# Kernel optimization log

Measured on AMD Instinct MI355X. Metric: run time of the kernel, lower is better.

The kernel has to match this reference:

```python
import jax, jax.numpy as jnp
import numpy as np

B, V, E = 2, 50000, 400000
FIN, COND, HID, OUT, ENC, EDG = 128, 32, 256, 128, 64, 16
EPS = 1e-5


def setup_inputs() -> dict:
    key = jax.random.key(0)
    ks = jax.random.split(key, 24)
    rn = lambda k, shp, s=0.05: jax.random.normal(k, shp, jnp.float32) * s
    return {
        "x": jax.random.normal(ks[0], (B, V, FIN), jnp.float32),
        "cond_x": jax.random.normal(ks[1], (V, COND), jnp.float32),
        "edge_attr": jax.random.normal(ks[2], (E, EDG), jnp.float32),
        "t": jax.random.normal(ks[3], (B, ENC), jnp.float32),
        "edge_index": jax.random.randint(ks[4], (2, E), 0, V, dtype=jnp.int32),
        # GCNConv weights (in, hid) + bias; Linear weights (hid, out) + bias
        "w_c0": rn(ks[5], (FIN + COND, HID)), "b_c0": rn(ks[6], (HID,)),
        "w_l0": rn(ks[7], (HID, HID)), "b_l0": rn(ks[8], (HID,)),
        "w_c1": rn(ks[9], (HID, HID)), "b_c1": rn(ks[10], (HID,)),
        "w_l1": rn(ks[11], (HID, HID)), "b_l1": rn(ks[12], (HID,)),
        "w_c2": rn(ks[13], (HID, HID)), "b_c2": rn(ks[14], (HID,)),
        "w_l2": rn(ks[15], (HID, OUT)), "b_l2": rn(ks[16], (OUT,)),
        "gn_g": jnp.ones((HID,), jnp.float32), "gn_b": jnp.zeros((HID,), jnp.float32),
        "film_w": rn(ks[17], (ENC, 2 * HID)), "film_b": rn(ks[18], (2 * HID,)),
    }


def _gcn(h, src, dst, dinv, W, b):
    # GCNConv: symmetric-normalized aggregation with self loops, then +bias.
    hw = h @ W  # (B, V, H)
    coef = (dinv[src] * dinv[dst])[None, :, None]            # (1, E, 1)
    self_loop = hw * (dinv * dinv)[None, :, None]            # norm of (i,i) edge
    agg = self_loop.at[:, dst, :].add(hw[:, src, :] * coef)  # scatter-add over dst
    return agg + b


def _groupnorm1(h, gamma, beta):
    # nn.GroupNorm(1, C) applied to (B, C, V): normalize over (C, V) per sample.
    mu = h.mean(axis=(1, 2), keepdims=True)
    var = ((h - mu) ** 2).mean(axis=(1, 2), keepdims=True)
    return (h - mu) * jax.lax.rsqrt(var + EPS) * gamma + beta


def reference(x, cond_x, edge_attr, t, edge_index,
              w_c0, b_c0, w_l0, b_l0, w_c1, b_c1, w_l1, b_l1,
              w_c2, b_c2, w_l2, b_l2, gn_g, gn_b, film_w, film_b):
    src, dst = edge_index[0], edge_index[1]
    deg = jnp.ones((V,), jnp.float32).at[dst].add(1.0)  # 1 = self loop
    dinv = jax.lax.rsqrt(deg)

    x_skip = x
    cond = jnp.broadcast_to(cond_x[None], (x.shape[0], V, COND))
    h = jnp.concatenate([x, cond], axis=-1)  # (B, V, FIN+COND)

    # layer 0: feature dim != hidden -> no norm
    h = jax.nn.relu(_gcn(h, src, dst, dinv, w_c0, b_c0))
    h = jax.nn.relu(h @ w_l0 + b_l0)  # dropout p=0 -> identity

    # layer 1: GroupNorm(1, hidden) then conv/linear
    h = _groupnorm1(h, gn_g, gn_b)
    h = jax.nn.relu(_gcn(h, src, dst, dinv, w_c1, b_c1))
    h = jax.nn.relu(h @ w_l1 + b_l1)

    # final gconv + FiLM + relu + linear + residual
    h = _gcn(h, src, dst, dinv, w_c2, b_c2)
    gb = t @ film_w + film_b                 # (B, 2*HID)
    gamma, beta = gb[:, :HID], gb[:, HID:]
    h = h * gamma[:, None, :] + beta[:, None, :]
    h = jax.nn.relu(h)
    out = h @ w_l2 + b_l2 + x_skip
    return out
```

## Files before the change

### kernel.cpp

```cpp
#include <hip/hip_runtime.h>
#include <stdint.h>

typedef unsigned short u16;
typedef short bf16x8 __attribute__((ext_vector_type(8)));
typedef float f32x4 __attribute__((ext_vector_type(4)));

constexpr int B_ = 2, V_ = 50000, E_ = 400000;
constexpr int FIN_ = 128, COND_ = 32, HID_ = 256, OUT_ = 128, ENC_ = 64;
constexpr int M_ = B_ * V_;
constexpr int MP_ = M_ + 256;
constexpr int K0_ = FIN_ + COND_;
constexpr float EPS_ = 1e-5f;

#define DEV static __device__ __forceinline__

DEV float b2f(u16 u) { union { float f; uint32_t i; } x; x.i = ((uint32_t)u) << 16; return x.f; }
DEV u16 f2b(float f) {
  union { float f; uint32_t i; } x; x.f = f;
  uint32_t r = x.i + 0x7fffu + ((x.i >> 16) & 1u);
  return (u16)(r >> 16);
}
DEV uint32_t pk2(float a, float b) { return (uint32_t)f2b(a) | ((uint32_t)f2b(b) << 16); }

#define GLDS16(gp, lp) __builtin_amdgcn_global_load_lds( \
    (const __attribute__((address_space(1))) void*)(gp), \
    (__attribute__((address_space(3))) void*)(lp), 16, 0, 0)

__global__ void k_count(const int* __restrict__ dst, int* __restrict__ cnt) {
  int e = blockIdx.x * blockDim.x + threadIdx.x;
  if (e < E_) atomicAdd(&cnt[dst[e]], 1);
}

__global__ void k_dinv(const int* __restrict__ cnt, float* __restrict__ dinv) {
  int v = blockIdx.x * blockDim.x + threadIdx.x;
  if (v < V_) dinv[v] = rsqrtf(1.0f + (float)cnt[v]);
}

__global__ __launch_bounds__(1024) void k_scan1(const int* __restrict__ cnt,
                                                int* __restrict__ tmp, int* __restrict__ bsum) {
  __shared__ int s[1024];
  int tid = threadIdx.x;
  int i = blockIdx.x * 1024 + tid;
  int v = (i < V_) ? cnt[i] : 0;
  s[tid] = v;
  __syncthreads();
  for (int off = 1; off < 1024; off <<= 1) {
    int t = (tid >= off) ? s[tid - off] : 0;
    __syncthreads();
    s[tid] += t;
    __syncthreads();
  }
  if (i < V_) tmp[i] = s[tid];
  if (tid == 1023) bsum[blockIdx.x] = s[1023];
}

__global__ void k_scan2(int* __restrict__ bsum, int n) {
  if (threadIdx.x == 0) {
    int a = 0;
    for (int i = 0; i < n; ++i) { a += bsum[i]; bsum[i] = a; }
  }
}

__global__ void k_scan3(const int* __restrict__ cnt, const int* __restrict__ tmp,
                        const int* __restrict__ bsum, int* __restrict__ row_ptr,
                        int* __restrict__ cursor) {
  int i = blockIdx.x * blockDim.x + threadIdx.x;
  if (i >= V_) return;
  int blk = i >> 10;
  int offs = blk ? bsum[blk - 1] : 0;
  int incl = tmp[i] + offs;
  row_ptr[i + 1] = incl;
  cursor[i] = incl - cnt[i];
  if (i == 0) row_ptr[0] = 0;
}

__global__ void k_fill(const int* __restrict__ src, const int* __restrict__ dst,
                       const float* __restrict__ dinv,
                       int* __restrict__ cursor, int2* __restrict__ csr) {
  int e = blockIdx.x * blockDim.x + threadIdx.x;
  if (e < E_) {
    int s = src[e], d = dst[e];
    int p = atomicAdd(&cursor[d], 1);
    float cf = dinv[s] * dinv[d];
    csr[p] = make_int2(s, __float_as_int(cf));
  }
}

__global__ void k_rowsum(const float* __restrict__ dinv, const int* __restrict__ row_ptr,
                         const int2* __restrict__ csr, float* __restrict__ rowsum) {
  int v = blockIdx.x * blockDim.x + threadIdx.x;
  if (v >= V_) return;
  float dv = dinv[v];
  float s = dv * dv;
  int e = row_ptr[v + 1];
  for (int j = row_ptr[v]; j < e; ++j) s += __int_as_float(csr[j].y);
  rowsum[v] = s;
}

__global__ void k_film(const float* __restrict__ t, const float* __restrict__ fw,
                       const float* __restrict__ fb, float* __restrict__ gb) {
  int b = blockIdx.x; int j = threadIdx.x;
  float acc = fb[j];
  for (int k = 0; k < ENC_; ++k) acc += t[b * ENC_ + k] * fw[k * 512 + j];
  gb[b * 512 + j] = acc;
}

__global__ void k_wconv(const float* __restrict__ W, u16* __restrict__ WT, int K, int N) {
  int idx = blockIdx.x * blockDim.x + threadIdx.x;
  if (idx < K * N) {
    int k = idx / N, n = idx % N;
    WT[n * K + k] = f2b(W[idx]);
  }
}

__global__ void k_wconv_g(const float* __restrict__ W, const float* __restrict__ gng,
                          u16* __restrict__ WT, int K, int N) {
  int idx = blockIdx.x * blockDim.x + threadIdx.x;
  if (idx < K * N) {
    int k = idx / N, n = idx % N;
    WT[n * K + k] = f2b(W[idx] * gng[k]);
  }
}

__global__ void k_gnreduce(const float4* __restrict__ part, int nblk,
                           float* __restrict__ stats) {
  int tid = threadIdx.x;
  float s0 = 0.f, ss0 = 0.f, s1 = 0.f, ss1 = 0.f;
  for (int i = tid; i < nblk; i += 256) {
    float4 p = part[i];
    s0 += p.x; ss0 += p.y; s1 += p.z; ss1 += p.w;
  }
  __shared__ float red[4][4];
#pragma unroll
  for (int o = 32; o > 0; o >>= 1) {
    s0  += __shfl_down(s0, o, 64);
    ss0 += __shfl_down(ss0, o, 64);
    s1  += __shfl_down(s1, o, 64);
    ss1 += __shfl_down(ss1, o, 64);
  }
  int w = tid >> 6, ln = tid & 63;
  if (ln == 0) { red[w][0] = s0; red[w][1] = ss0; red[w][2] = s1; red[w][3] = ss1; }
  __syncthreads();
  if (tid == 0) {
    float S0 = red[0][0] + red[1][0] + red[2][0] + red[3][0];
    float SS0 = red[0][1] + red[1][1] + red[2][1] + red[3][1];
    float S1 = red[0][2] + red[1][2] + red[2][2] + red[3][2];
    float SS1 = red[0][3] + red[1][3] + red[2][3] + red[3][3];
    float n = (float)V_ * (float)HID_;
    float mu0 = S0 / n, var0 = SS0 / n - mu0 * mu0;
    float mu1 = S1 / n, var1 = SS1 / n - mu1 * mu1;
    stats[0] = mu0; stats[1] = rsqrtf(var0 + EPS_);
    stats[2] = mu1; stats[3] = rsqrtf(var1 + EPS_);
  }
}

__global__ void k_gnfold(const float* __restrict__ gng, const float* __restrict__ gnb,
                         const float* __restrict__ W, const float* __restrict__ stats,
                         float* __restrict__ kc) {
  int n = blockIdx.x, c = threadIdx.x;
  float wv = W[c * HID_ + n];
  float gw = gng[c] * wv, bw = gnb[c] * wv;
  __shared__ float sg[4], sb[4];
#pragma unroll
  for (int o = 32; o > 0; o >>= 1) {
    gw += __shfl_down(gw, o, 64);
    bw += __shfl_down(bw, o, 64);
  }
  int w = c >> 6, ln = c & 63;
  if (ln == 0) { sg[w] = gw; sb[w] = bw; }
  __syncthreads();
  if (c == 0) {
    float G = sg[0] + sg[1] + sg[2] + sg[3];
    float Bw = sb[0] + sb[1] + sb[2] + sb[3];
    for (int b = 0; b < B_; ++b)
      kc[b * HID_ + n] = Bw - stats[b * 2] * stats[b * 2 + 1] * G;
  }
}

__global__ void k_prep0(const float* __restrict__ x, const float* __restrict__ cond,
                        u16* __restrict__ A0) {
  int idx = blockIdx.x * blockDim.x + threadIdx.x;
  if (idx >= M_ * K0_ / 4) return;
  int e = idx * 4;
  int r = e / K0_, c = e % K0_;
  float4 v;
  if (c < FIN_) v = *(const float4*)&x[(size_t)r * FIN_ + c];
  else { int vv = r % V_; v = *(const float4*)&cond[(size_t)vv * COND_ + (c - FIN_)]; }
  uint2 o;
  o.x = pk2(v.x, v.y);
  o.y = pk2(v.z, v.w);
  *(uint2*)&A0[e] = o;
}

template<int KW>
__global__ __launch_bounds__(256) void k_gather(
    const u16* __restrict__ hw, const float* __restrict__ dinv,
    const int* __restrict__ row_ptr, const int2* __restrict__ csr,
    u16* __restrict__ out)
{
  __shared__ f32x4 redA[3][2][32];
  __shared__ f32x4 redB[3][2][32];
  const int v   = blockIdx.x;
  const int tid = threadIdx.x;
  const int nb  = tid >> 6;
  const int b   = (tid >> 5) & 1;
  const int l   = tid & 31;
  const int c0  = l * 8;
  const bool act = l < (KW / 8);

  const float dv = dinv[v];
  const int beg = row_ptr[v], end = row_ptr[v + 1];

  float acc[8];
#pragma unroll
  for (int k = 0; k < 8; ++k) acc[k] = 0.f;

  if (act) {
    int j = beg + nb;
    for (; j + 4 < end; j += 8) {
      int2 e0 = csr[j];
      int2 e1 = csr[j + 4];
      float cf0 = __int_as_float(e0.y);
      float cf1 = __int_as_float(e1.y);
      uint4 u0 = *(const uint4*)&hw[((size_t)b * V_ + e0.x) * KW + c0];
      uint4 u1 = *(const uint4*)&hw[((size_t)b * V_ + e1.x) * KW + c0];
      u16 a0[8]; *(uint4*)a0 = u0;
      u16 a1[8]; *(uint4*)a1 = u1;
#pragma unroll
      for (int k = 0; k < 8; ++k) acc[k] += b2f(a0[k]) * cf0;
#pragma unroll
      for (int k = 0; k < 8; ++k) acc[k] += b2f(a1[k]) * cf1;
    }
    if (j < end) {
      int2 e0 = csr[j];
      float cf0 = __int_as_float(e0.y);
      uint4 u0 = *(const uint4*)&hw[((size_t)b * V_ + e0.x) * KW + c0];
      u16 a0[8]; *(uint4*)a0 = u0;
#pragma unroll
      for (int k = 0; k < 8; ++k) acc[k] += b2f(a0[k]) * cf0;
    }
  }

  if (nb > 0) {
    redA[nb - 1][b][l] = f32x4{acc[0], acc[1], acc[2], acc[3]};
    redB[nb - 1][b][l] = f32x4{acc[4], acc[5], acc[6], acc[7]};
  }
  __syncthreads();
  if (nb == 0 && act) {
#pragma unroll
    for (int g = 0; g < 3; ++g) {
      f32x4 ra = redA[g][b][l], rb = redB[g][b][l];
      acc[0] += ra[0]; acc[1] += ra[1]; acc[2] += ra[2]; acc[3] += ra[3];
      acc[4] += rb[0]; acc[5] += rb[1]; acc[6] += rb[2]; acc[7] += rb[3];
    }
    float sl = dv * dv;
    uint4 u = *(const uint4*)&hw[((size_t)b * V_ + v) * KW + c0];
    u16 us[8]; *(uint4*)us = u;
#pragma unroll
    for (int k = 0; k < 8; ++k) acc[k] += b2f(us[k]) * sl;
    uint4 o;
    o.x = pk2(acc[0], acc[1]);
    o.y = pk2(acc[2], acc[3]);
    o.z = pk2(acc[4], acc[5]);
    o.w = pk2(acc[6], acc[7]);
    *(uint4*)&out[((size_t)b * V_ + v) * KW + c0] = o;
  }
}

template<int P1E, int P2E, int K1, int N2>
__global__ __launch_bounds__(256) void k_pair(
    const u16* __restrict__ A, const u16* __restrict__ W1T, const u16* __restrict__ W2T,
    const float* __restrict__ b1, const float* __restrict__ b2,
    const float* __restrict__ stats, const float* __restrict__ kc,
    const float* __restrict__ rowsum, const float* __restrict__ gb,
    const float* __restrict__ xres, float4* __restrict__ part,
    void* __restrict__ Out)
{
  constexpr int BM = 64, BK = 32, N1 = 256;
  constexpr int FN2 = N2 / 64;
  __shared__ alignas(16) u16 Asg[BM * BK];
  __shared__ alignas(16) u16 Bsg[N1 * BK];
  __shared__ alignas(16) u16 T1[BM * N1];
  __shared__ float sred[4][4];
  const int tile_m = blockIdx.x * BM;
  const int tid = threadIdx.x;
  const int wave = tid >> 6, lane = tid & 63;
  const int lr = lane & 15, lkg = lane >> 4;
  const int phys = lkg ^ ((lr >> 1) & 3);

  f32x4 acc[4][4];
#pragma unroll
  for (int i = 0; i < 4; ++i)
#pragma unroll
    for (int j = 0; j < 4; ++j) acc[i][j] = {0.f, 0.f, 0.f, 0.f};

  for (int kb = 0; kb < K1; kb += BK) {
    {
      int row = tid >> 2;
      int sslot = (tid & 3) ^ ((row >> 1) & 3);
      GLDS16(A + (size_t)(tile_m + row) * K1 + kb + sslot * 8, &Asg[(wave * 64) * 8]);
    }
#pragma unroll
    for (int it = 0; it < 4; ++it) {
      int c = tid + it * 256;
      int row = c >> 2;
      int sslot = (c & 3) ^ ((row >> 1) & 3);
      GLDS16(W1T + (size_t)row * K1 + kb + sslot * 8, &Bsg[(it * 256 + wave * 64) * 8]);
    }
    __syncthreads();
    bf16x8 af[4], bf[4];
#pragma unroll
    for (int fm = 0; fm < 4; ++fm) af[fm] = *(const bf16x8*)&Asg[(fm * 16 + lr) * BK + phys * 8];
#pragma unroll
    for (int fn = 0; fn < 4; ++fn) bf[fn] = *(const bf16x8*)&Bsg[(wave * 64 + fn * 16 + lr) * BK + phys * 8];
#pragma unroll
    for (int fm = 0; fm < 4; ++fm)
#pragma unroll
      for (int fn = 0; fn < 4; ++fn)
        acc[fm][fn] = __builtin_amdgcn_mfma_f32_16x16x32_bf16(bf[fn], af[fm], acc[fm][fn], 0, 0, 0);
    __syncthreads();
  }

#pragma unroll
  for (int fm = 0; fm < 4; ++fm) {
    const int row = fm * 16 + lr;
    const int gr = tile_m + row;
    const int bb = (gr >= V_) ? 1 : 0;
    float rsc = 1.f, rsum = 0.f;
    if (P1E == 1) {
      rsc = stats[bb * 2 + 1];
      int node = (gr < M_) ? (gr - bb * V_) : 0;
      rsum = rowsum[node];
    }
#pragma unroll
    for (int fn = 0; fn < 4; ++fn) {
      const int colb = wave * 64 + fn * 16 + lkg * 4;
      float v0 = acc[fm][fn][0], v1 = acc[fm][fn][1];
      float v2 = acc[fm][fn][2], v3 = acc[fm][fn][3];
      float4 bs = *(const float4*)&b1[colb];
      if (P1E == 0) {
        v0 = fmaxf(v0 + bs.x, 0.f); v1 = fmaxf(v1 + bs.y, 0.f);
        v2 = fmaxf(v2 + bs.z, 0.f); v3 = fmaxf(v3 + bs.w, 0.f);
      }
      if (P1E == 1) {
        float4 kcv = *(const float4*)&kc[bb * 256 + colb];
        v0 = fmaxf(v0 * rsc + rsum * kcv.x + bs.x, 0.f);
        v1 = fmaxf(v1 * rsc + rsum * kcv.y + bs.y, 0.f);
        v2 = fmaxf(v2 * rsc + rsum * kcv.z + bs.z, 0.f);
        v3 = fmaxf(v3 * rsc + rsum * kcv.w + bs.w, 0.f);
      }
      if (P1E == 2) {
        float4 g = *(const float4*)&gb[bb * 512 + colb];
        float4 be = *(const float4*)&gb[bb * 512 + 256 + colb];
        v0 = fmaxf((v0 + bs.x) * g.x + be.x, 0.f);
        v1 = fmaxf((v1 + bs.y) * g.y + be.y, 0.f);
        v2 = fmaxf((v2 + bs.z) * g.z + be.z, 0.f);
        v3 = fmaxf((v3 + bs.w) * g.w + be.w, 0.f);
      }
      int pg = (colb >> 2) ^ ((row & 7) << 1);
      uint2 o; o.x = pk2(v0, v1); o.y = pk2(v2, v3);
      *(uint2*)&T1[row * 256 + pg * 4] = o;
    }
  }
  __syncthreads();

  f32x4 acc2[4][FN2];
#pragma unroll
  for (int i = 0; i < 4; ++i)
#pragma unroll
    for (int j = 0; j < FN2; ++j) acc2[i][j] = {0.f, 0.f, 0.f, 0.f};

  for (int kb2 = 0; kb2 < 256; kb2 += BK) {
#pragma unroll
    for (int it = 0; it < FN2; ++it) {
      int c = tid + it * 256;
      int row = c >> 2;
      int sslot = (c & 3) ^ ((row >> 1) & 3);
      GLDS16(W2T + (size_t)row * 256 + kb2 + sslot * 8, &Bsg[(it * 256 + wave * 64) * 8]);
    }
    __syncthreads();
    bf16x8 af2[4], bf2[FN2];
#pragma unroll
    for (int fm = 0; fm < 4; ++fm) {
      int row = fm * 16 + lr;
      int pg = ((kb2 >> 2) + lkg * 2) ^ ((row & 7) << 1);
      af2[fm] = *(const bf16x8*)&T1[row * 256 + pg * 4];
    }
#pragma unroll
    for (int fn = 0; fn < FN2; ++fn)
      bf2[fn] = *(const bf16x8*)&Bsg[(wave * (N2 / 4) + fn * 16 + lr) * BK + phys * 8];
#pragma unroll
    for (int fm = 0; fm < 4; ++fm)
#pragma unroll
      for (int fn = 0; fn < FN2; ++fn)
        acc2[fm][fn] = __builtin_amdgcn_mfma_f32_16x16x32_bf16(bf2[fn], af2[fm], acc2[fm][fn], 0, 0, 0);
    __syncthreads();
  }

  float s0 = 0.f, ss0 = 0.f, s1 = 0.f, ss1 = 0.f;
#pragma unroll
  for (int fm = 0; fm < 4; ++fm) {
    const int row = tile_m + fm * 16 + lr;
    if (row >= M_) continue;
#pragma unroll
    for (int fn = 0; fn < FN2; ++fn) {
      const int colb = wave * (N2 / 4) + fn * 16 + lkg * 4;
      float v0 = acc2[fm][fn][0], v1 = acc2[fm][fn][1];
      float v2 = acc2[fm][fn][2], v3 = acc2[fm][fn][3];
      float4 bs = *(const float4*)&b2[colb];
      if (P2E == 0 || P2E == 1) {
        v0 = fmaxf(v0 + bs.x, 0.f); v1 = fmaxf(v1 + bs.y, 0.f);
        v2 = fmaxf(v2 + bs.z, 0.f); v3 = fmaxf(v3 + bs.w, 0.f);
        if (P2E == 1) {
          if (row >= V_) { s1 += v0 + v1 + v2 + v3; ss1 += v0*v0 + v1*v1 + v2*v2 + v3*v3; }
          else           { s0 += v0 + v1 + v2 + v3; ss0 += v0*v0 + v1*v1 + v2*v2 + v3*v3; }
        }
        uint2 o; o.x = pk2(v0, v1); o.y = pk2(v2, v3);
        *(uint2*)&((u16*)Out)[(size_t)row * N2 + colb] = o;
      } else {
        float4 xr = *(const float4*)&xres[(size_t)row * N2 + colb];
        float4 o;
        o.x = v0 + bs.x + xr.x; o.y = v1 + bs.y + xr.y;
        o.z = v2 + bs.z + xr.z; o.w = v3 + bs.w + xr.w;
        *(float4*)&((float*)Out)[(size_t)row * N2 + colb] = o;
      }
    }
  }
  if (P2E == 1) {
#pragma unroll
    for (int o = 32; o > 0; o >>= 1) {
      s0  += __shfl_down(s0, o, 64);
      ss0 += __shfl_down(ss0, o, 64);
      s1  += __shfl_down(s1, o, 64);
      ss1 += __shfl_down(ss1, o, 64);
    }
    if (lane == 0) { sred[wave][0] = s0; sred[wave][1] = ss0; sred[wave][2] = s1; sred[wave][3] = ss1; }
    __syncthreads();
    if (tid == 0) {
      float4 p;
      p.x = sred[0][0] + sred[1][0] + sred[2][0] + sred[3][0];
      p.y = sred[0][1] + sred[1][1] + sred[2][1] + sred[3][1];
      p.z = sred[0][2] + sred[1][2] + sred[2][2] + sred[3][2];
      p.w = sred[0][3] + sred[1][3] + sred[2][3] + sred[3][3];
      part[blockIdx.x] = p;
    }
  }
}

extern "C" void kernel_launch(void* const* d_in, const int* in_sizes, int n_in,
                              void* d_out, int out_size, void* d_ws, size_t ws_size,
                              hipStream_t stream) {
  (void)in_sizes; (void)n_in; (void)out_size; (void)ws_size;
  const float* x      = (const float*)d_in[0];
  const float* cond_x = (const float*)d_in[1];
  const float* t      = (const float*)d_in[3];
  const int*   ei     = (const int*)d_in[4];
  const float* w_c0 = (const float*)d_in[5];  const float* b_c0 = (const float*)d_in[6];
  const float* w_l0 = (const float*)d_in[7];  const float* b_l0 = (const float*)d_in[8];
  const float* w_c1 = (const float*)d_in[9];  const float* b_c1 = (const float*)d_in[10];
  const float* w_l1 = (const float*)d_in[11]; const float* b_l1 = (const float*)d_in[12];
  const float* w_c2 = (const float*)d_in[13]; const float* b_c2 = (const float*)d_in[14];
  const float* w_l2 = (const float*)d_in[15]; const float* b_l2 = (const float*)d_in[16];
  const float* gn_g = (const float*)d_in[17]; const float* gn_b = (const float*)d_in[18];
  const float* film_w = (const float*)d_in[19]; const float* film_b = (const float*)d_in[20];

  char* wsp = (char*)d_ws;
  size_t off = 0;
  auto alloc = [&](size_t bytes) -> char* {
    char* p = wsp + off; off += (bytes + 255) & ~(size_t)255; return p;
  };
  constexpr int GM64 = (M_ + 63) / 64;
  int*   cnt       = (int*)  alloc((size_t)V_ * 4);
  int*   row_ptr   = (int*)  alloc((size_t)(V_ + 1) * 4);
  int*   cursor    = (int*)  alloc((size_t)V_ * 4);
  int2*  csr       = (int2*) alloc((size_t)E_ * 8);
  int*   scan_tmp  = (int*)  alloc((size_t)V_ * 4);
  int*   scan_bsum = (int*)  alloc(64 * 4);
  float* dinv      = (float*)alloc((size_t)V_ * 4);
  float* rowsum    = (float*)alloc((size_t)V_ * 4);
  float* stats     = (float*)alloc(16);
  float4* part     = (float4*)alloc((size_t)GM64 * 16);
  float* gb        = (float*)alloc(2 * 512 * 4);
  float* kc        = (float*)alloc(2 * HID_ * 4);
  u16* wc0T  = (u16*)alloc((size_t)256 * 160 * 2);
  u16* wl0T  = (u16*)alloc((size_t)256 * 256 * 2);
  u16* wc1Tg = (u16*)alloc((size_t)256 * 256 * 2);
  u16* wl1T  = (u16*)alloc((size_t)256 * 256 * 2);
  u16* wc2T  = (u16*)alloc((size_t)256 * 256 * 2);
  u16* wl2T  = (u16*)alloc((size_t)128 * 256 * 2);
  u16* A0    = (u16*)alloc((size_t)MP_ * K0_ * 2);
  u16* HA0   = (u16*)alloc((size_t)MP_ * K0_ * 2);
  u16* HB    = (u16*)alloc((size_t)MP_ * HID_ * 2);
  u16* HA1   = (u16*)alloc((size_t)MP_ * HID_ * 2);

  const int* srcI = ei;
  const int* dstI = ei + E_;

  hipMemsetAsync(cnt, 0, (size_t)V_ * 4, stream);

  constexpr int NBLK = (V_ + 1023) / 1024;
  k_count<<<dim3((E_ + 255) / 256), dim3(256), 0, stream>>>(dstI, cnt);
  k_dinv <<<dim3((V_ + 255) / 256), dim3(256), 0, stream>>>(cnt, dinv);
  k_scan1<<<dim3(NBLK), dim3(1024), 0, stream>>>(cnt, scan_tmp, scan_bsum);
  k_scan2<<<dim3(1), dim3(64), 0, stream>>>(scan_bsum, NBLK);
  k_scan3<<<dim3((V_ + 255) / 256), dim3(256), 0, stream>>>(cnt, scan_tmp, scan_bsum, row_ptr, cursor);
  k_fill <<<dim3((E_ + 255) / 256), dim3(256), 0, stream>>>(srcI, dstI, dinv, cursor, csr);
  k_rowsum<<<dim3((V_ + 255) / 256), dim3(256), 0, stream>>>(dinv, row_ptr, csr, rowsum);
  k_film <<<dim3(2), dim3(512), 0, stream>>>(t, film_w, film_b, gb);

  k_wconv  <<<dim3((160 * 256 + 255) / 256), dim3(256), 0, stream>>>(w_c0, wc0T, 160, 256);
  k_wconv  <<<dim3((256 * 256 + 255) / 256), dim3(256), 0, stream>>>(w_l0, wl0T, 256, 256);
  k_wconv_g<<<dim3((256 * 256 + 255) / 256), dim3(256), 0, stream>>>(w_c1, gn_g, wc1Tg, 256, 256);
  k_wconv  <<<dim3((256 * 256 + 255) / 256), dim3(256), 0, stream>>>(w_l1, wl1T, 256, 256);
  k_wconv  <<<dim3((256 * 256 + 255) / 256), dim3(256), 0, stream>>>(w_c2, wc2T, 256, 256);
  k_wconv  <<<dim3((256 * 128 + 255) / 256), dim3(256), 0, stream>>>(w_l2, wl2T, 256, 128);

  k_prep0<<<dim3(M_ * K0_ / 4 / 256), dim3(256), 0, stream>>>(x, cond_x, A0);

  k_gather<160><<<dim3(V_), 256, 0, stream>>>(A0, dinv, row_ptr, csr, HA0);
  k_pair<0, 1, 160, 256><<<dim3(GM64), 256, 0, stream>>>(
      HA0, wc0T, wl0T, b_c0, b_l0, nullptr, nullptr, nullptr, nullptr, nullptr, part, HB);

  k_gnreduce<<<dim3(1), dim3(256), 0, stream>>>(part, GM64, stats);
  k_gnfold <<<dim3(256), dim3(256), 0, stream>>>(gn_g, gn_b, w_c1, stats, kc);

  k_gather<256><<<dim3(V_), 256, 0, stream>>>(HB, dinv, row_ptr, csr, HA1);
  k_pair<1, 0, 256, 256><<<dim3(GM64), 256, 0, stream>>>(
      HA1, wc1Tg, wl1T, b_c1, b_l1, stats, kc, rowsum, nullptr, nullptr, nullptr, HB);

  k_gather<256><<<dim3(V_), 256, 0, stream>>>(HB, dinv, row_ptr, csr, HA1);
  k_pair<2, 2, 256, 128><<<dim3(GM64), 256, 0, stream>>>(
      HA1, wc2T, wl2T, b_c2, b_l2, nullptr, nullptr, nullptr, gb, x, nullptr, (void*)d_out);
}
```

Measured before the change: 515.5 us.

## Interleave batch dimension into node rows so gathers fetch both batches together

Reorders the internal activation layout from batch-major (b*V+v) to node-major interleaved (v*2+b) across the input prep, the gather/aggregation kernel and the fused GEMM epilogues. The two batch copies of a neighbor's features become adjacent in memory, so each edge's gather touches contiguous lines instead of two far-apart rows, which should improve cache and DRAM locality for the scatter-gather. GroupNorm statistics and row scaling now select the batch from row parity, and the final output is written back in the original batch-major layout.

Result: slower. 556.8 us (+8.0%).

```diff
diff --git a/kernel.cpp b/kernel.cpp
--- a/kernel.cpp
+++ b/kernel.cpp
@@ -183,12 +183,13 @@
   if (idx >= M_ * K0_ / 4) return;
   int e = idx * 4;
   int r = e / K0_, c = e % K0_;
-  float4 v;
-  if (c < FIN_) v = *(const float4*)&x[(size_t)r * FIN_ + c];
-  else { int vv = r % V_; v = *(const float4*)&cond[(size_t)vv * COND_ + (c - FIN_)]; }
+  int b = r & 1, v = r >> 1;
+  float4 w;
+  if (c < FIN_) w = *(const float4*)&x[((size_t)b * V_ + v) * FIN_ + c];
+  else w = *(const float4*)&cond[(size_t)v * COND_ + (c - FIN_)];
   uint2 o;
-  o.x = pk2(v.x, v.y);
-  o.y = pk2(v.z, v.w);
+  o.x = pk2(w.x, w.y);
+  o.y = pk2(w.z, w.w);
   *(uint2*)&A0[e] = o;
 }
 
@@ -222,8 +223,8 @@
       int2 e1 = csr[j + 4];
       float cf0 = __int_as_float(e0.y);
       float cf1 = __int_as_float(e1.y);
-      uint4 u0 = *(const uint4*)&hw[((size_t)b * V_ + e0.x) * KW + c0];
-      uint4 u1 = *(const uint4*)&hw[((size_t)b * V_ + e1.x) * KW + c0];
+      uint4 u0 = *(const uint4*)&hw[((size_t)e0.x * 2 + b) * KW + c0];
+      uint4 u1 = *(const uint4*)&hw[((size_t)e1.x * 2 + b) * KW + c0];
       u16 a0[8]; *(uint4*)a0 = u0;
       u16 a1[8]; *(uint4*)a1 = u1;
 #pragma unroll
@@ -234,7 +235,7 @@
     if (j < end) {
       int2 e0 = csr[j];
       float cf0 = __int_as_float(e0.y);
-      uint4 u0 = *(const uint4*)&hw[((size_t)b * V_ + e0.x) * KW + c0];
+      uint4 u0 = *(const uint4*)&hw[((size_t)e0.x * 2 + b) * KW + c0];
       u16 a0[8]; *(uint4*)a0 = u0;
 #pragma unroll
       for (int k = 0; k < 8; ++k) acc[k] += b2f(a0[k]) * cf0;
@@ -254,7 +255,7 @@
       acc[4] += rb[0]; acc[5] += rb[1]; acc[6] += rb[2]; acc[7] += rb[3];
     }
     float sl = dv * dv;
-    uint4 u = *(const uint4*)&hw[((size_t)b * V_ + v) * KW + c0];
+    uint4 u = *(const uint4*)&hw[((size_t)v * 2 + b) * KW + c0];
     u16 us[8]; *(uint4*)us = u;
 #pragma unroll
     for (int k = 0; k < 8; ++k) acc[k] += b2f(us[k]) * sl;
@@ -263,7 +264,7 @@
     o.y = pk2(acc[2], acc[3]);
     o.z = pk2(acc[4], acc[5]);
     o.w = pk2(acc[6], acc[7]);
-    *(uint4*)&out[((size_t)b * V_ + v) * KW + c0] = o;
+    *(uint4*)&out[((size_t)v * 2 + b) * KW + c0] = o;
   }
 }
 
@@ -325,11 +326,11 @@
   for (int fm = 0; fm < 4; ++fm) {
     const int row = fm * 16 + lr;
     const int gr = tile_m + row;
-    const int bb = (gr >= V_) ? 1 : 0;
+    const int bb = gr & 1;
     float rsc = 1.f, rsum = 0.f;
     if (P1E == 1) {
       rsc = stats[bb * 2 + 1];
-      int node = (gr < M_) ? (gr - bb * V_) : 0;
+      int node = (gr < M_) ? (gr >> 1) : 0;
       rsum = rowsum[node];
     }
 #pragma unroll
@@ -412,17 +413,19 @@
         v0 = fmaxf(v0 + bs.x, 0.f); v1 = fmaxf(v1 + bs.y, 0.f);
         v2 = fmaxf(v2 + bs.z, 0.f); v3 = fmaxf(v3 + bs.w, 0.f);
         if (P2E == 1) {
-          if (row >= V_) { s1 += v0 + v1 + v2 + v3; ss1 += v0*v0 + v1*v1 + v2*v2 + v3*v3; }
-          else           { s0 += v0 + v1 + v2 + v3; ss0 += v0*v0 + v1*v1 + v2*v2 + v3*v3; }
+          if (row & 1) { s1 += v0 + v1 + v2 + v3; ss1 += v0*v0 + v1*v1 + v2*v2 + v3*v3; }
+          else         { s0 += v0 + v1 + v2 + v3; ss0 += v0*v0 + v1*v1 + v2*v2 + v3*v3; }
         }
         uint2 o; o.x = pk2(v0, v1); o.y = pk2(v2, v3);
         *(uint2*)&((u16*)Out)[(size_t)row * N2 + colb] = o;
       } else {
-        float4 xr = *(const float4*)&xres[(size_t)row * N2 + colb];
+        const int node = row >> 1, bb = row & 1;
+        const size_t gidx = ((size_t)bb * V_ + node) * N2 + colb;
+        float4 xr = *(const float4*)&xres[gidx];
         float4 o;
         o.x = v0 + bs.x + xr.x; o.y = v1 + bs.y + xr.y;
         o.z = v2 + bs.z + xr.z; o.w = v3 + bs.w + xr.w;
-        *(float4*)&((float*)Out)[(size_t)row * N2 + colb] = o;
+        *(float4*)&((float*)Out)[gidx] = o;
       }
     }
   }
```

## Load GEMM operands directly from global memory instead of staging through LDS

Applied to the files above, without the earlier changes.

The fused pair-GEMM kernel stops staging A and weight tiles into shared memory with global_load_lds, and each wave now loads its MFMA fragments straight from global memory into registers. This drops the two __syncthreads per K step and frees the LDS that held the staging buffers, which may raise occupancy. In exchange, the four waves in a block each reload the shared A rows, and all blocks reload weights from L2/L1 without reuse through LDS, so memory traffic and latency exposure go up.

New measurement: 580.9 us. 12.7% more time.

```diff
diff --git a/kernel.cpp b/kernel.cpp
--- a/kernel.cpp
+++ b/kernel.cpp
@@ -21,10 +21,6 @@
   return (u16)(r >> 16);
 }
 DEV uint32_t pk2(float a, float b) { return (uint32_t)f2b(a) | ((uint32_t)f2b(b) << 16); }
-
-#define GLDS16(gp, lp) __builtin_amdgcn_global_load_lds( \
-    (const __attribute__((address_space(1))) void*)(gp), \
-    (__attribute__((address_space(3))) void*)(lp), 16, 0, 0)
 
 __global__ void k_count(const int* __restrict__ dst, int* __restrict__ cnt) {
   int e = blockIdx.x * blockDim.x + threadIdx.x;
@@ -276,17 +272,14 @@
     const float* __restrict__ xres, float4* __restrict__ part,
     void* __restrict__ Out)
 {
-  constexpr int BM = 64, BK = 32, N1 = 256;
+  constexpr int BM = 64, N1 = 256;
   constexpr int FN2 = N2 / 64;
-  __shared__ alignas(16) u16 Asg[BM * BK];
-  __shared__ alignas(16) u16 Bsg[N1 * BK];
   __shared__ alignas(16) u16 T1[BM * N1];
   __shared__ float sred[4][4];
   const int tile_m = blockIdx.x * BM;
   const int tid = threadIdx.x;
   const int wave = tid >> 6, lane = tid & 63;
   const int lr = lane & 15, lkg = lane >> 4;
-  const int phys = lkg ^ ((lr >> 1) & 3);
 
   f32x4 acc[4][4];
 #pragma unroll
@@ -294,31 +287,19 @@
 #pragma unroll
     for (int j = 0; j < 4; ++j) acc[i][j] = {0.f, 0.f, 0.f, 0.f};
 
-  for (int kb = 0; kb < K1; kb += BK) {
-    {
-      int row = tid >> 2;
-      int sslot = (tid & 3) ^ ((row >> 1) & 3);
-      GLDS16(A + (size_t)(tile_m + row) * K1 + kb + sslot * 8, &Asg[(wave * 64) * 8]);
-    }
-#pragma unroll
-    for (int it = 0; it < 4; ++it) {
-      int c = tid + it * 256;
-      int row = c >> 2;
-      int sslot = (c & 3) ^ ((row >> 1) & 3);
-      GLDS16(W1T + (size_t)row * K1 + kb + sslot * 8, &Bsg[(it * 256 + wave * 64) * 8]);
-    }
-    __syncthreads();
+  for (int kb = 0; kb < K1; kb += 32) {
     bf16x8 af[4], bf[4];
 #pragma unroll
-    for (int fm = 0; fm < 4; ++fm) af[fm] = *(const bf16x8*)&Asg[(fm * 16 + lr) * BK + phys * 8];
-#pragma unroll
-    for (int fn = 0; fn < 4; ++fn) bf[fn] = *(const bf16x8*)&Bsg[(wave * 64 + fn * 16 + lr) * BK + phys * 8];
+    for (int fm = 0; fm < 4; ++fm)
+      af[fm] = *(const bf16x8*)&A[(size_t)(tile_m + fm * 16 + lr) * K1 + kb + lkg * 8];
+#pragma unroll
+    for (int fn = 0; fn < 4; ++fn)
+      bf[fn] = *(const bf16x8*)&W1T[(size_t)(wave * 64 + fn * 16 + lr) * K1 + kb + lkg * 8];
 #pragma unroll
     for (int fm = 0; fm < 4; ++fm)
 #pragma unroll
       for (int fn = 0; fn < 4; ++fn)
         acc[fm][fn] = __builtin_amdgcn_mfma_f32_16x16x32_bf16(bf[fn], af[fm], acc[fm][fn], 0, 0, 0);
-    __syncthreads();
   }
 
 #pragma unroll
@@ -370,15 +351,7 @@
 #pragma unroll
     for (int j = 0; j < FN2; ++j) acc2[i][j] = {0.f, 0.f, 0.f, 0.f};
 
-  for (int kb2 = 0; kb2 < 256; kb2 += BK) {
-#pragma unroll
-    for (int it = 0; it < FN2; ++it) {
-      int c = tid + it * 256;
-      int row = c >> 2;
-      int sslot = (c & 3) ^ ((row >> 1) & 3);
-      GLDS16(W2T + (size_t)row * 256 + kb2 + sslot * 8, &Bsg[(it * 256 + wave * 64) * 8]);
-    }
-    __syncthreads();
+  for (int kb2 = 0; kb2 < 256; kb2 += 32) {
     bf16x8 af2[4], bf2[FN2];
 #pragma unroll
     for (int fm = 0; fm < 4; ++fm) {
@@ -388,13 +361,12 @@
     }
 #pragma unroll
     for (int fn = 0; fn < FN2; ++fn)
-      bf2[fn] = *(const bf16x8*)&Bsg[(wave * (N2 / 4) + fn * 16 + lr) * BK + phys * 8];
+      bf2[fn] = *(const bf16x8*)&W2T[(size_t)(wave * (N2 / 4) + fn * 16 + lr) * 256 + kb2 + lkg * 8];
 #pragma unroll
     for (int fm = 0; fm < 4; ++fm)
 #pragma unroll
       for (int fn = 0; fn < FN2; ++fn)
         acc2[fm][fn] = __builtin_amdgcn_mfma_f32_16x16x32_bf16(bf2[fn], af2[fm], acc2[fm][fn], 0, 0, 0);
-    __syncthreads();
   }
 
   float s0 = 0.f, ss0 = 0.f, s1 = 0.f, ss1 = 0.f;
```
